# Optimization experiments

Measured on AMD Instinct MI355X. Metric: run time of the kernel, lower is better.

The kernel has to match this reference:

```python
import jax, jax.numpy as jnp
import numpy as np

D_MODEL = 1024
NUM_HEADS = 16
THETA = 10000.0
BATCH = 2
SEQ = 2048


def setup_inputs() -> dict:
    key = jax.random.key(0)
    ks = jax.random.split(key, 5)
    std = (2.0 / (D_MODEL + D_MODEL)) ** 0.5
    mk = lambda k: jax.random.truncated_normal(k, -3.0, 3.0, (D_MODEL, D_MODEL), jnp.float32) * std
    return {
        'x': jax.random.normal(ks[0], (BATCH, SEQ, D_MODEL), jnp.float32),
        'Wq': mk(ks[1]),
        'Wk': mk(ks[2]),
        'Wv': mk(ks[3]),
        'Wo': mk(ks[4]),
        'token_positions': jnp.arange(SEQ, dtype=jnp.int32),
    }


def _apply_rope(x, token_positions, theta):
    # x: (B, H, S, d_k)
    d_k = x.shape[-1]
    freq = 1.0 / theta ** (jnp.arange(0, d_k, 2, dtype=jnp.float32) / d_k)  # (d_k//2,)
    freqs = token_positions.astype(jnp.float32)[:, None] * freq[None, :]   # (S, d_k//2)
    cos, sin = jnp.cos(freqs), jnp.sin(freqs)
    x_real = x[..., 0::2]
    x_imag = x[..., 1::2]
    rot_real = x_real * cos - x_imag * sin
    rot_imag = x_real * sin + x_imag * cos
    # interleave back: (..., d_k//2, 2) -> (..., d_k)
    out = jnp.stack([rot_real, rot_imag], axis=-1)
    return out.reshape(x.shape)


def reference(x, Wq, Wk, Wv, Wo, token_positions):
    B, S, D = x.shape
    H = NUM_HEADS
    d_k = D // H

    def split_heads(t):
        return t.reshape(B, S, H, d_k).transpose(0, 2, 1, 3)  # (B, H, S, d_k)

    Q = split_heads(jnp.einsum('bsd,od->bso', x, Wq))
    K = split_heads(jnp.einsum('bsd,od->bso', x, Wk))
    V = split_heads(jnp.einsum('bsd,od->bso', x, Wv))

    Q = _apply_rope(Q, token_positions, THETA)
    K = _apply_rope(K, token_positions, THETA)

    # naive materialized attention with causal mask, faithful to source
    scores = jnp.einsum('bhqd,bhkd->bhqk', Q, K)
    causal = jnp.tril(jnp.ones((S, S), dtype=bool))  # True = attend
    scores = jnp.where(causal[None, None], scores, -jnp.inf)
    scores = scores / jnp.sqrt(jnp.asarray(d_k, scores.dtype))
    probs = jax.nn.softmax(scores, axis=-1)
    attn = jnp.einsum('bhqk,bhkd->bhqd', probs, V)  # (B, H, S, d_v)

    attn = attn.transpose(0, 2, 1, 3).reshape(B, S, D)
    return jnp.einsum('bsd,od->bso', attn, Wo)
```

## Files before the change

### kernel.cpp

```cpp
#include <hip/hip_runtime.h>
#include <hip/hip_bf16.h>
#include <math.h>

#define NUM_HEADS 16
#define DK 64
#define SEQ 2048
#define BATCHN 2
#define DM 1024
#define BS (BATCHN*SEQ)
#define LSCALE 0.18033688011112042f

typedef __bf16 bf16x8 __attribute__((ext_vector_type(8)));
typedef float floatx4 __attribute__((ext_vector_type(4)));
typedef unsigned short ushort;
typedef unsigned int uint;

__device__ __forceinline__ ushort f2bu(float f){
    union { __hip_bfloat16 h; ushort u; } cv; cv.h = __float2bfloat16(f); return cv.u;
}
__device__ __forceinline__ uint packbf(float a, float b){
    return (uint)f2bu(a) | ((uint)f2bu(b) << 16);
}
__device__ __forceinline__ float bu2f(ushort u){
    union { uint u; float f; } cv; cv.u = (uint)u << 16; return cv.f;
}
__device__ __forceinline__ void gl16(const void* g, void* l){
    __builtin_amdgcn_global_load_lds(
        (const __attribute__((address_space(1))) unsigned int*)g,
        (__attribute__((address_space(3))) unsigned int*)l, 16, 0, 0);
}

__global__ __launch_bounds__(256)
void castall(const float* __restrict__ x,  const float* __restrict__ wq,
             const float* __restrict__ wk, const float* __restrict__ wv,
             const float* __restrict__ wo, const int* __restrict__ pos,
             ushort* __restrict__ xb, ushort* __restrict__ wqkb,
             ushort* __restrict__ wvb, ushort* __restrict__ wob,
             float2* __restrict__ tab)
{
    int bid = blockIdx.x;
    if (bid >= 4096) {
        int idx = (bid - 4096)*256 + threadIdx.x;
        int s = idx >> 5, i = idx & 31;
        float invf = expf(-0.28782313662425575f * (float)i);
        float ang = (float)pos[s] * invf;
        float sn, cs; sincosf(ang, &sn, &cs);
        tab[idx] = make_float2(cs, sn);
        return;
    }
    const float* src; ushort* dst; int off;
    if (bid < 2048)      { src = x;  dst = xb;             off = bid; }
    else if (bid < 2560) { src = wq; dst = wqkb;           off = bid - 2048; }
    else if (bid < 3072) { src = wk; dst = wqkb + 1048576; off = bid - 2560; }
    else if (bid < 3584) { src = wv; dst = wvb;            off = bid - 3072; }
    else                 { src = wo; dst = wob;            off = bid - 3584; }
    int i = off*2048 + threadIdx.x*8;
    float4 a = *(const float4*)(src+i);
    float4 b = *(const float4*)(src+i+4);
    uint4 o;
    o.x = packbf(a.x, a.y);
    o.y = packbf(a.z, a.w);
    o.z = packbf(b.x, b.y);
    o.w = packbf(b.z, b.w);
    *(uint4*)(dst+i) = o;
}

__global__ __launch_bounds__(256)
void proj_fused(const ushort* __restrict__ xb, const ushort* __restrict__ Wqkb,
                const ushort* __restrict__ Wvb, ushort* __restrict__ Qb,
                ushort* __restrict__ VTp, const float2* __restrict__ rope)
{
    __shared__ ushort As[128][32];
    __shared__ ushort Bs[128][32];

    const int bid = blockIdx.x;
    const ushort* A; const ushort* W; int row0, col0, mode;
    if (bid < 512) { A = xb;  W = Wqkb; row0 = (bid >> 4) * 128;
                     col0 = (bid & 15) * 128;  mode = 1; }
    else           { int i = bid - 512; A = Wvb; W = xb;
                     row0 = (i >> 5) * 128; col0 = (i & 31) * 128; mode = 2; }

    const int t = threadIdx.x;
    const int w = t >> 6;
    const int L = t & 63;
    const int lr = L & 15;
    const int lq = L >> 4;
    const int wrow = w * 32;

    floatx4 acc[2][8];
    #pragma unroll
    for (int i = 0; i < 2; ++i)
        #pragma unroll
        for (int j = 0; j < 8; ++j)
            acc[i][j] = (floatx4){0.f,0.f,0.f,0.f};

    const int rr = t >> 2, ko = (t & 3) * 8;
    const ushort* ga = A + (size_t)(row0 + rr) * DM + ko;
    const ushort* gb = W + (size_t)(col0 + rr) * DM + ko;

    for (int k0 = 0; k0 < DM; k0 += 32) {
        __syncthreads();
        gl16(ga + k0,                    &As[rr][ko]);
        gl16(ga + k0 + (size_t)64*DM,    &As[rr + 64][ko]);
        gl16(gb + k0,                    &Bs[rr][ko]);
        gl16(gb + k0 + (size_t)64*DM,    &Bs[rr + 64][ko]);
        __syncthreads();

        bf16x8 aF0 = *(const bf16x8*)&As[wrow + lr][lq*8];
        bf16x8 aF1 = *(const bf16x8*)&As[wrow + 16 + lr][lq*8];
        #pragma unroll
        for (int tc = 0; tc < 8; ++tc) {
            bf16x8 bF = *(const bf16x8*)&Bs[tc*16 + lr][lq*8];
            acc[0][tc] = __builtin_amdgcn_mfma_f32_16x16x32_bf16(aF0, bF, acc[0][tc], 0, 0, 0);
            acc[1][tc] = __builtin_amdgcn_mfma_f32_16x16x32_bf16(aF1, bF, acc[1][tc], 0, 0, 0);
        }
    }

    if (mode == 2) {
        #pragma unroll
        for (int tr = 0; tr < 2; ++tr)
            #pragma unroll
            for (int tc = 0; tc < 8; ++tc)
                #pragma unroll
                for (int r = 0; r < 4; ++r) {
                    int m = row0 + wrow + tr*16 + lq*4 + r;
                    int c = col0 + tc*16 + lr;
                    VTp[(size_t)m * BS + c] = f2bu(acc[tr][tc][r]);
                }
    } else {
        const int mat = col0 >> 10;
        const int base_hh = (col0 & 1023) >> 6;
        ushort* out = Qb + (size_t)mat * (BATCHN*NUM_HEADS*SEQ*DK);
        const float qscale = mat ? 1.f : LSCALE;
        #pragma unroll
        for (int tr = 0; tr < 2; ++tr)
            #pragma unroll
            for (int tc = 0; tc < 8; ++tc)
                #pragma unroll
                for (int r = 0; r < 4; ++r) {
                    int m = row0 + wrow + tr*16 + lq*4 + r;
                    int b = m >> 11;
                    int s = m & (SEQ - 1);
                    int dd = (tc*16 + lr) & 63;
                    int hh = base_hh + (tc >> 2);
                    float v = acc[tr][tc][r];
                    float o = __shfl_xor(v, 1, 64);
                    float2 cs = rope[s*32 + (dd >> 1)];
                    float rv = (dd & 1) ? fmaf(o, cs.y,  v * cs.x)
                                        : fmaf(-o, cs.y, v * cs.x);
                    out[((size_t)((b*NUM_HEADS + hh)*SEQ + s))*DK + dd] =
                        f2bu(rv * qscale);
                }
    }
}

__global__ __launch_bounds__(256)
void gemm_out(const ushort* __restrict__ A, const ushort* __restrict__ W,
              float* __restrict__ out)
{
    __shared__ ushort As[128][32];
    __shared__ ushort Bs[64][32];

    const int t = threadIdx.x;
    const int w = t >> 6;
    const int L = t & 63;
    const int lr = L & 15;
    const int lq = L >> 4;
    const int row0 = blockIdx.y * 128;
    const int col0 = blockIdx.x * 64;
    const int wrow = w * 32;

    floatx4 acc[2][4];
    #pragma unroll
    for (int i = 0; i < 2; ++i)
        #pragma unroll
        for (int j = 0; j < 4; ++j)
            acc[i][j] = (floatx4){0.f,0.f,0.f,0.f};

    const int rr = t >> 2, ko = (t & 3) * 8;
    const ushort* ga = A + (size_t)(row0 + rr) * DM + ko;
    const ushort* gb = W + (size_t)(col0 + rr) * DM + ko;

    for (int k0 = 0; k0 < DM; k0 += 32) {
        __syncthreads();
        gl16(ga + k0,                 &As[rr][ko]);
        gl16(ga + k0 + (size_t)64*DM, &As[rr + 64][ko]);
        gl16(gb + k0,                 &Bs[rr][ko]);
        __syncthreads();

        bf16x8 aF0 = *(const bf16x8*)&As[wrow + lr][lq*8];
        bf16x8 aF1 = *(const bf16x8*)&As[wrow + 16 + lr][lq*8];
        #pragma unroll
        for (int tc = 0; tc < 4; ++tc) {
            bf16x8 bF = *(const bf16x8*)&Bs[tc*16 + lr][lq*8];
            acc[0][tc] = __builtin_amdgcn_mfma_f32_16x16x32_bf16(aF0, bF, acc[0][tc], 0, 0, 0);
            acc[1][tc] = __builtin_amdgcn_mfma_f32_16x16x32_bf16(aF1, bF, acc[1][tc], 0, 0, 0);
        }
    }

    #pragma unroll
    for (int tr = 0; tr < 2; ++tr)
        #pragma unroll
        for (int tc = 0; tc < 4; ++tc)
            #pragma unroll
            for (int r = 0; r < 4; ++r) {
                int m = row0 + wrow + tr*16 + lq*4 + r;
                int c = col0 + tc*16 + lr;
                out[(size_t)m * DM + c] = acc[tr][tc][r];
            }
}

__global__ __launch_bounds__(256)
void attn_mfma(const ushort* __restrict__ Qb, const ushort* __restrict__ Kb,
               const ushort* __restrict__ VT, ushort* __restrict__ attnb,
               ushort* __restrict__ Opart, float* __restrict__ lpart)
{
    __shared__ ushort Ks[64][72];
    __shared__ ushort Vs[64][72];
    __shared__ ushort Ps[4][16][72];

    const int t = threadIdx.x;
    const int w = t >> 6;
    const int L = t & 63;
    const int lr = L & 15, lq = L >> 4;
    const int h  = blockIdx.y;
    const int b  = blockIdx.z;

    int qt, chunk, nch;
    {
        const int bx = blockIdx.x;
        if (bx < 8)       { qt = bx;              chunk = 0;     nch = 1; }
        else if (bx < 24) { int i = bx - 8;  qt = 8  + (i>>1); chunk = i&1;        nch = 2; }
        else if (bx < 48) { int i = bx - 24; int q3 = i/3; qt = 16 + q3; chunk = i - q3*3; nch = 3; }
        else              { int i = bx - 48; qt = 24 + (i>>2); chunk = i&3;        nch = 4; }
    }
    const int nt = qt + 1;
    const int t0 = (nt * chunk) / nch;
    const int t1 = (nt * (chunk + 1)) / nch;
    const int q0 = qt * 64;
    const int qw = q0 + w * 16;
    const size_t qkbase = (size_t)(b*NUM_HEADS + h) * SEQ * DK;

    bf16x8 qF0, qF1;
    {
        const ushort* qp = Qb + qkbase + (size_t)(qw + lr) * DK + lq*8;
        qF0 = *(const bf16x8*)qp;
        qF1 = *(const bf16x8*)(qp + 32);
    }

    floatx4 O[4];
    #pragma unroll
    for (int g = 0; g < 4; ++g) O[g] = (floatx4){0.f,0.f,0.f,0.f};
    float l_lane = 0.f;

    const int sr = t >> 3, sc = (t & 7) * 8;
    const ushort* kp0 = Kb + qkbase + (size_t)sr * DK + sc;
    const ushort* vp0 = VT + ((size_t)(h*DK + sr)) * BS + b*SEQ + sc;

    uint4 k0v, k1v, v0v, v1v;
    {
        const int kb = t0 * 64;
        k0v = *(const uint4*)(kp0 + (size_t)kb * DK);
        k1v = *(const uint4*)(kp0 + (size_t)(kb + 32) * DK);
        v0v = *(const uint4*)(vp0 + kb);
        v1v = *(const uint4*)(vp0 + (size_t)32 * BS + kb);
    }

    for (int tile = t0; tile < t1; ++tile) {
        const int kb = tile * 64;
        __syncthreads();
        *(uint4*)&Ks[sr][sc]      = k0v;
        *(uint4*)&Ks[sr + 32][sc] = k1v;
        *(uint4*)&Vs[sr][sc]      = v0v;
        *(uint4*)&Vs[sr + 32][sc] = v1v;
        __syncthreads();

        if (tile + 1 < t1) {
            const int kb2 = kb + 64;
            k0v = *(const uint4*)(kp0 + (size_t)kb2 * DK);
            k1v = *(const uint4*)(kp0 + (size_t)(kb2 + 32) * DK);
            v0v = *(const uint4*)(vp0 + kb2);
            v1v = *(const uint4*)(vp0 + (size_t)32 * BS + kb2);
        }

        const bool lastt = (tile == nt - 1);
        const int lim = qw + lr - kb;

        #pragma unroll
        for (int g = 0; g < 4; ++g) {
            floatx4 s = (floatx4){0.f,0.f,0.f,0.f};
            bf16x8 kf0 = *(const bf16x8*)&Ks[g*16 + lr][lq*8];
            bf16x8 kf1 = *(const bf16x8*)&Ks[g*16 + lr][32 + lq*8];
            s = __builtin_amdgcn_mfma_f32_16x16x32_bf16(kf0, qF0, s, 0, 0, 0);
            s = __builtin_amdgcn_mfma_f32_16x16x32_bf16(kf1, qF1, s, 0, 0, 0);
            float p0, p1, p2, p3;
            if (lastt) {
                const int kbase = g*16 + lq*4;
                p0 = (kbase + 0 <= lim) ? exp2f(s[0]) : 0.f;
                p1 = (kbase + 1 <= lim) ? exp2f(s[1]) : 0.f;
                p2 = (kbase + 2 <= lim) ? exp2f(s[2]) : 0.f;
                p3 = (kbase + 3 <= lim) ? exp2f(s[3]) : 0.f;
            } else {
                p0 = exp2f(s[0]); p1 = exp2f(s[1]);
                p2 = exp2f(s[2]); p3 = exp2f(s[3]);
            }
            l_lane += (p0 + p1) + (p2 + p3);
            uint2 pk;
            pk.x = packbf(p0, p1);
            pk.y = packbf(p2, p3);
            *(uint2*)&Ps[w][lr][g*16 + lq*4] = pk;
        }
        asm volatile("s_waitcnt lgkmcnt(0)" ::: "memory");

        #pragma unroll
        for (int c = 0; c < 2; ++c) {
            bf16x8 pF = *(const bf16x8*)&Ps[w][lr][c*32 + lq*8];
            #pragma unroll
            for (int g2 = 0; g2 < 4; ++g2) {
                bf16x8 vf = *(const bf16x8*)&Vs[g2*16 + lr][c*32 + lq*8];
                O[g2] = __builtin_amdgcn_mfma_f32_16x16x32_bf16(pF, vf, O[g2], 0, 0, 0);
            }
        }
    }

    l_lane += __shfl_xor(l_lane, 16, 64);
    l_lane += __shfl_xor(l_lane, 32, 64);

    if (nch == 1) {
        #pragma unroll
        for (int r = 0; r < 4; ++r) {
            float lv = __shfl(l_lane, lq*4 + r, 64);
            float li = 1.f / lv;
            int s = qw + lq*4 + r;
            #pragma unroll
            for (int g2 = 0; g2 < 4; ++g2)
                attnb[((size_t)(b*SEQ + s))*DM + h*DK + g2*16 + lr] = f2bu(O[g2][r] * li);
        }
    } else {
        const int slot = ((b*NUM_HEADS + h)*24 + (qt - 8))*4 + chunk;
        ushort* Op = Opart + (size_t)slot * 4096;
        #pragma unroll
        for (int r = 0; r < 4; ++r) {
            int ql = w*16 + lq*4 + r;
            #pragma unroll
            for (int g2 = 0; g2 < 4; ++g2)
                Op[ql*64 + g2*16 + lr] = f2bu(O[g2][r]);
        }
        if (lq == 0) lpart[(size_t)slot*64 + w*16 + lr] = l_lane;
    }
}

__global__ __launch_bounds__(256)
void combine(const ushort* __restrict__ Opart, const float* __restrict__ lpart,
             ushort* __restrict__ attnb)
{
    int gx = blockIdx.x;
    int qti = gx % 24, bh = gx / 24;
    int h = bh & 15, b = bh >> 4;
    int qt = 8 + qti;
    int nch = (qt >> 3) + 1;
    int tid = threadIdx.x;
    int row = tid >> 2, c0 = (tid & 3) * 16;
    const int base_slot = (bh*24 + qti)*4;

    float acc[16];
    #pragma unroll
    for (int e = 0; e < 16; ++e) acc[e] = 0.f;
    float l = 0.f;

    for (int c = 0; c < nch; ++c) {
        const ushort* Op = Opart + (size_t)(base_slot + c)*4096 + row*64 + c0;
        uint4 u0 = *(const uint4*)(Op);
        uint4 u1 = *(const uint4*)(Op + 8);
        const ushort* h0 = (const ushort*)&u0;
        const ushort* h1 = (const ushort*)&u1;
        #pragma unroll
        for (int e = 0; e < 8; ++e) { acc[e]   += bu2f(h0[e]); }
        #pragma unroll
        for (int e = 0; e < 8; ++e) { acc[8+e] += bu2f(h1[e]); }
        l += lpart[(size_t)(base_slot + c)*64 + row];
    }
    float li = 1.f / l;
    int s = qt*64 + row;
    ushort* dst = attnb + ((size_t)(b*SEQ + s))*DM + h*DK + c0;
    #pragma unroll
    for (int e = 0; e < 16; ++e) dst[e] = f2bu(acc[e] * li);
}

extern "C" void kernel_launch(void* const* d_in, const int* in_sizes, int n_in,
                              void* d_out, int out_size, void* d_ws, size_t ws_size,
                              hipStream_t stream) {
    const float* x   = (const float*)d_in[0];
    const float* Wq  = (const float*)d_in[1];
    const float* Wk  = (const float*)d_in[2];
    const float* Wv  = (const float*)d_in[3];
    const float* Wo  = (const float*)d_in[4];
    const int*   pos = (const int*)d_in[5];
    float* out = (float*)d_out;

    const size_t MB = 1u << 20;
    char* ws = (char*)d_ws;
    ushort* xb    = (ushort*)(ws);
    ushort* Wqkb  = (ushort*)(ws +  8*MB);
    ushort* Wvb   = (ushort*)(ws + 12*MB);
    ushort* Opart = (ushort*)(ws);
    float*  lpart = (float*)(ws + 24*MB);
    ushort* Qb    = (ushort*)(ws + 25*MB);
    ushort* Kb    = (ushort*)(ws + 33*MB);
    ushort* VT    = (ushort*)(ws + 41*MB);
    ushort* attnb = (ushort*)(ws + 49*MB);
    float2* ropeT = (float2*)(ws + 57*MB);
    ushort* Wob   = (ushort*)(ws + 58*MB);

    dim3 blk(256);
    castall<<<4352, blk, 0, stream>>>(x, Wq, Wk, Wv, Wo, pos,
                                      xb, Wqkb, Wvb, Wob, ropeT);

    proj_fused<<<768, blk, 0, stream>>>(xb, Wqkb, Wvb, Qb, VT, ropeT);

    attn_mfma<<<dim3(80, NUM_HEADS, BATCHN), blk, 0, stream>>>(Qb, Kb, VT, attnb,
                                                               Opart, lpart);
    combine<<<768, blk, 0, stream>>>(Opart, lpart, attnb);

    gemm_out<<<dim3(16,32), blk, 0, stream>>>(attnb, Wob, out);
}
```

Measured before the change: 204.4 us.

## Restructure attention to 2 waves with 32 query rows each, register-resident P and swizzled LDS

The attention kernel now runs 128 threads per block, with each wave handling 32 query rows (two 16-row MFMA tiles). This halves the LDS reads of K and V per query row. The probability tile is packed straight into MFMA A-operand registers instead of going through a shared-memory Ps buffer. K and V tiles are stored in LDS with an XOR swizzle in place of padding, and V is stored in a permuted column order that matches the P register layout. The register prefetch of the next tile is dropped in favour of loading inside the loop, which risks exposing global load latency, and fewer waves per block may reduce latency hiding.

```diff
diff --git a/kernel.cpp b/kernel.cpp
--- a/kernel.cpp
+++ b/kernel.cpp
@@ -210,14 +210,13 @@
             }
 }
 
-__global__ __launch_bounds__(256)
+__global__ __launch_bounds__(128)
 void attn_mfma(const ushort* __restrict__ Qb, const ushort* __restrict__ Kb,
                const ushort* __restrict__ VT, ushort* __restrict__ attnb,
                ushort* __restrict__ Opart, float* __restrict__ lpart)
 {
-    __shared__ ushort Ks[64][72];
-    __shared__ ushort Vs[64][72];
-    __shared__ ushort Ps[4][16][72];
+    __shared__ ushort Ks[64*64];
+    __shared__ ushort Vs[64*64];
 
     const int t = threadIdx.x;
     const int w = t >> 6;
@@ -238,115 +237,157 @@
     const int t0 = (nt * chunk) / nch;
     const int t1 = (nt * (chunk + 1)) / nch;
     const int q0 = qt * 64;
-    const int qw = q0 + w * 16;
+    const int qw = q0 + w * 32;
     const size_t qkbase = (size_t)(b*NUM_HEADS + h) * SEQ * DK;
 
-    bf16x8 qF0, qF1;
+    bf16x8 qA0, qA1, qB0, qB1;
     {
         const ushort* qp = Qb + qkbase + (size_t)(qw + lr) * DK + lq*8;
-        qF0 = *(const bf16x8*)qp;
-        qF1 = *(const bf16x8*)(qp + 32);
-    }
-
-    floatx4 O[4];
-    #pragma unroll
-    for (int g = 0; g < 4; ++g) O[g] = (floatx4){0.f,0.f,0.f,0.f};
-    float l_lane = 0.f;
-
-    const int sr = t >> 3, sc = (t & 7) * 8;
-    const ushort* kp0 = Kb + qkbase + (size_t)sr * DK + sc;
-    const ushort* vp0 = VT + ((size_t)(h*DK + sr)) * BS + b*SEQ + sc;
-
-    uint4 k0v, k1v, v0v, v1v;
-    {
-        const int kb = t0 * 64;
-        k0v = *(const uint4*)(kp0 + (size_t)kb * DK);
-        k1v = *(const uint4*)(kp0 + (size_t)(kb + 32) * DK);
-        v0v = *(const uint4*)(vp0 + kb);
-        v1v = *(const uint4*)(vp0 + (size_t)32 * BS + kb);
-    }
+        qA0 = *(const bf16x8*)qp;
+        qA1 = *(const bf16x8*)(qp + 32);
+        qB0 = *(const bf16x8*)(qp + 16*DK);
+        qB1 = *(const bf16x8*)(qp + 16*DK + 32);
+    }
+
+    floatx4 O0[4], O1[4];
+    #pragma unroll
+    for (int g = 0; g < 4; ++g) {
+        O0[g] = (floatx4){0.f,0.f,0.f,0.f};
+        O1[g] = (floatx4){0.f,0.f,0.f,0.f};
+    }
+    float l0 = 0.f, l1 = 0.f;
+
+    const int sr = t >> 3, t7 = t & 7;
+    const int kwb  = (sr*64 + t7*8) ^ ((sr & 7) << 3);
+    const int pc0  = ((t7 >> 2) << 3) | ((t7 & 1) << 2) | ((t7 >> 1) & 1);
+    const int vwb0 = (sr*64 + pc0*4)     ^ ((sr & 7) << 3);
+    const int vwb1 = (sr*64 + pc0*4 + 8) ^ ((sr & 7) << 3);
+    const ushort* kpt = Kb + qkbase + (size_t)sr * DK + t7*8;
+    const ushort* vpt = VT + ((size_t)(h*DK + sr)) * BS + b*SEQ + t7*8;
+
+    const int kro0 = (lr*64 + lq*8)      ^ ((lr & 7) << 3);
+    const int kro1 = (lr*64 + 32 + lq*8) ^ ((lr & 7) << 3);
 
     for (int tile = t0; tile < t1; ++tile) {
         const int kb = tile * 64;
-        __syncthreads();
-        *(uint4*)&Ks[sr][sc]      = k0v;
-        *(uint4*)&Ks[sr + 32][sc] = k1v;
-        *(uint4*)&Vs[sr][sc]      = v0v;
-        *(uint4*)&Vs[sr + 32][sc] = v1v;
-        __syncthreads();
-
-        if (tile + 1 < t1) {
-            const int kb2 = kb + 64;
-            k0v = *(const uint4*)(kp0 + (size_t)kb2 * DK);
-            k1v = *(const uint4*)(kp0 + (size_t)(kb2 + 32) * DK);
-            v0v = *(const uint4*)(vp0 + kb2);
-            v1v = *(const uint4*)(vp0 + (size_t)32 * BS + kb2);
-        }
+        const ushort* kg = kpt + (size_t)kb * DK;
+        const ushort* vg = vpt + kb;
+        uint4 kv0 = *(const uint4*)(kg);
+        uint4 kv1 = *(const uint4*)(kg + 16*DK);
+        uint4 kv2 = *(const uint4*)(kg + 32*DK);
+        uint4 kv3 = *(const uint4*)(kg + 48*DK);
+        uint4 vv0 = *(const uint4*)(vg);
+        uint4 vv1 = *(const uint4*)(vg + (size_t)16*BS);
+        uint4 vv2 = *(const uint4*)(vg + (size_t)32*BS);
+        uint4 vv3 = *(const uint4*)(vg + (size_t)48*BS);
+        __syncthreads();
+        *(uint4*)&Ks[kwb]        = kv0;
+        *(uint4*)&Ks[kwb + 1024] = kv1;
+        *(uint4*)&Ks[kwb + 2048] = kv2;
+        *(uint4*)&Ks[kwb + 3072] = kv3;
+        *(uint2*)&Vs[vwb0]        = make_uint2(vv0.x, vv0.y);
+        *(uint2*)&Vs[vwb1]        = make_uint2(vv0.z, vv0.w);
+        *(uint2*)&Vs[vwb0 + 1024] = make_uint2(vv1.x, vv1.y);
+        *(uint2*)&Vs[vwb1 + 1024] = make_uint2(vv1.z, vv1.w);
+        *(uint2*)&Vs[vwb0 + 2048] = make_uint2(vv2.x, vv2.y);
+        *(uint2*)&Vs[vwb1 + 2048] = make_uint2(vv2.z, vv2.w);
+        *(uint2*)&Vs[vwb0 + 3072] = make_uint2(vv3.x, vv3.y);
+        *(uint2*)&Vs[vwb1 + 3072] = make_uint2(vv3.z, vv3.w);
+        __syncthreads();
 
         const bool lastt = (tile == nt - 1);
-        const int lim = qw + lr - kb;
-
+        const int lim0 = qw + lr - kb;
+        const int lim1 = lim0 + 16;
+
+        uint2 pk0[4], pk1[4];
         #pragma unroll
         for (int g = 0; g < 4; ++g) {
-            floatx4 s = (floatx4){0.f,0.f,0.f,0.f};
-            bf16x8 kf0 = *(const bf16x8*)&Ks[g*16 + lr][lq*8];
-            bf16x8 kf1 = *(const bf16x8*)&Ks[g*16 + lr][32 + lq*8];
-            s = __builtin_amdgcn_mfma_f32_16x16x32_bf16(kf0, qF0, s, 0, 0, 0);
-            s = __builtin_amdgcn_mfma_f32_16x16x32_bf16(kf1, qF1, s, 0, 0, 0);
+            bf16x8 kf0 = *(const bf16x8*)&Ks[kro0 + g*1024];
+            bf16x8 kf1 = *(const bf16x8*)&Ks[kro1 + g*1024];
+            floatx4 s0 = (floatx4){0.f,0.f,0.f,0.f};
+            s0 = __builtin_amdgcn_mfma_f32_16x16x32_bf16(kf0, qA0, s0, 0, 0, 0);
+            s0 = __builtin_amdgcn_mfma_f32_16x16x32_bf16(kf1, qA1, s0, 0, 0, 0);
+            floatx4 s1 = (floatx4){0.f,0.f,0.f,0.f};
+            s1 = __builtin_amdgcn_mfma_f32_16x16x32_bf16(kf0, qB0, s1, 0, 0, 0);
+            s1 = __builtin_amdgcn_mfma_f32_16x16x32_bf16(kf1, qB1, s1, 0, 0, 0);
+            const int kbase = g*16 + lq*4;
             float p0, p1, p2, p3;
             if (lastt) {
-                const int kbase = g*16 + lq*4;
-                p0 = (kbase + 0 <= lim) ? exp2f(s[0]) : 0.f;
-                p1 = (kbase + 1 <= lim) ? exp2f(s[1]) : 0.f;
-                p2 = (kbase + 2 <= lim) ? exp2f(s[2]) : 0.f;
-                p3 = (kbase + 3 <= lim) ? exp2f(s[3]) : 0.f;
+                p0 = (kbase + 0 <= lim0) ? exp2f(s0[0]) : 0.f;
+                p1 = (kbase + 1 <= lim0) ? exp2f(s0[1]) : 0.f;
+                p2 = (kbase + 2 <= lim0) ? exp2f(s0[2]) : 0.f;
+                p3 = (kbase + 3 <= lim0) ? exp2f(s0[3]) : 0.f;
             } else {
-                p0 = exp2f(s[0]); p1 = exp2f(s[1]);
-                p2 = exp2f(s[2]); p3 = exp2f(s[3]);
-            }
-            l_lane += (p0 + p1) + (p2 + p3);
-            uint2 pk;
-            pk.x = packbf(p0, p1);
-            pk.y = packbf(p2, p3);
-            *(uint2*)&Ps[w][lr][g*16 + lq*4] = pk;
-        }
-        asm volatile("s_waitcnt lgkmcnt(0)" ::: "memory");
+                p0 = exp2f(s0[0]); p1 = exp2f(s0[1]);
+                p2 = exp2f(s0[2]); p3 = exp2f(s0[3]);
+            }
+            l0 += (p0 + p1) + (p2 + p3);
+            pk0[g] = make_uint2(packbf(p0, p1), packbf(p2, p3));
+            if (lastt) {
+                p0 = (kbase + 0 <= lim1) ? exp2f(s1[0]) : 0.f;
+                p1 = (kbase + 1 <= lim1) ? exp2f(s1[1]) : 0.f;
+                p2 = (kbase + 2 <= lim1) ? exp2f(s1[2]) : 0.f;
+                p3 = (kbase + 3 <= lim1) ? exp2f(s1[3]) : 0.f;
+            } else {
+                p0 = exp2f(s1[0]); p1 = exp2f(s1[1]);
+                p2 = exp2f(s1[2]); p3 = exp2f(s1[3]);
+            }
+            l1 += (p0 + p1) + (p2 + p3);
+            pk1[g] = make_uint2(packbf(p0, p1), packbf(p2, p3));
+        }
 
         #pragma unroll
         for (int c = 0; c < 2; ++c) {
-            bf16x8 pF = *(const bf16x8*)&Ps[w][lr][c*32 + lq*8];
+            union { uint u[4]; bf16x8 v; } a0, a1;
+            a0.u[0] = pk0[2*c].x;   a0.u[1] = pk0[2*c].y;
+            a0.u[2] = pk0[2*c+1].x; a0.u[3] = pk0[2*c+1].y;
+            a1.u[0] = pk1[2*c].x;   a1.u[1] = pk1[2*c].y;
+            a1.u[2] = pk1[2*c+1].x; a1.u[3] = pk1[2*c+1].y;
+            const int vro = c ? kro1 : kro0;
             #pragma unroll
             for (int g2 = 0; g2 < 4; ++g2) {
-                bf16x8 vf = *(const bf16x8*)&Vs[g2*16 + lr][c*32 + lq*8];
-                O[g2] = __builtin_amdgcn_mfma_f32_16x16x32_bf16(pF, vf, O[g2], 0, 0, 0);
-            }
-        }
-    }
-
-    l_lane += __shfl_xor(l_lane, 16, 64);
-    l_lane += __shfl_xor(l_lane, 32, 64);
+                bf16x8 vf = *(const bf16x8*)&Vs[vro + g2*1024];
+                O0[g2] = __builtin_amdgcn_mfma_f32_16x16x32_bf16(a0.v, vf, O0[g2], 0, 0, 0);
+                O1[g2] = __builtin_amdgcn_mfma_f32_16x16x32_bf16(a1.v, vf, O1[g2], 0, 0, 0);
+            }
+        }
+    }
+
+    l0 += __shfl_xor(l0, 16, 64);
+    l0 += __shfl_xor(l0, 32, 64);
+    l1 += __shfl_xor(l1, 16, 64);
+    l1 += __shfl_xor(l1, 32, 64);
 
     if (nch == 1) {
         #pragma unroll
         for (int r = 0; r < 4; ++r) {
-            float lv = __shfl(l_lane, lq*4 + r, 64);
-            float li = 1.f / lv;
-            int s = qw + lq*4 + r;
-            #pragma unroll
-            for (int g2 = 0; g2 < 4; ++g2)
-                attnb[((size_t)(b*SEQ + s))*DM + h*DK + g2*16 + lr] = f2bu(O[g2][r] * li);
+            float li0 = 1.f / __shfl(l0, lq*4 + r, 64);
+            float li1 = 1.f / __shfl(l1, lq*4 + r, 64);
+            int s0r = qw + lq*4 + r;
+            int s1r = qw + 16 + lq*4 + r;
+            #pragma unroll
+            for (int g2 = 0; g2 < 4; ++g2) {
+                attnb[((size_t)(b*SEQ + s0r))*DM + h*DK + g2*16 + lr] = f2bu(O0[g2][r] * li0);
+                attnb[((size_t)(b*SEQ + s1r))*DM + h*DK + g2*16 + lr] = f2bu(O1[g2][r] * li1);
+            }
         }
     } else {
         const int slot = ((b*NUM_HEADS + h)*24 + (qt - 8))*4 + chunk;
         ushort* Op = Opart + (size_t)slot * 4096;
         #pragma unroll
         for (int r = 0; r < 4; ++r) {
-            int ql = w*16 + lq*4 + r;
-            #pragma unroll
-            for (int g2 = 0; g2 < 4; ++g2)
-                Op[ql*64 + g2*16 + lr] = f2bu(O[g2][r]);
-        }
-        if (lq == 0) lpart[(size_t)slot*64 + w*16 + lr] = l_lane;
+            int ql0 = w*32 + lq*4 + r;
+            int ql1 = w*32 + 16 + lq*4 + r;
+            #pragma unroll
+            for (int g2 = 0; g2 < 4; ++g2) {
+                Op[ql0*64 + g2*16 + lr] = f2bu(O0[g2][r]);
+                Op[ql1*64 + g2*16 + lr] = f2bu(O1[g2][r]);
+            }
+        }
+        if (lq == 0) {
+            lpart[(size_t)slot*64 + w*32 + lr]      = l0;
+            lpart[(size_t)slot*64 + w*32 + 16 + lr] = l1;
+        }
     }
 }
 
@@ -418,8 +459,8 @@
 
     proj_fused<<<768, blk, 0, stream>>>(xb, Wqkb, Wvb, Qb, VT, ropeT);
 
-    attn_mfma<<<dim3(80, NUM_HEADS, BATCHN), blk, 0, stream>>>(Qb, Kb, VT, attnb,
-                                                               Opart, lpart);
+    attn_mfma<<<dim3(80, NUM_HEADS, BATCHN), dim3(128), 0, stream>>>(Qb, Kb, VT, attnb,
+                                                                     Opart, lpart);
     combine<<<768, blk, 0, stream>>>(Opart, lpart, attnb);
 
     gemm_out<<<dim3(16,32), blk, 0, stream>>>(attnb, Wob, out);
```

Measured after the change: 207.2 us. Within noise of the previous version (+1.4%).
